# Performance work log

Hardware: AMD Instinct MI355X
Metric: run time of the kernel (lower is better)

## Reference

```python
import jax, jax.numpy as jnp
import numpy as np

EMBED_DIM = 1280
NUM_HEADS = 20
HEAD_DIM = EMBED_DIM // NUM_HEADS


def setup_inputs() -> dict:
    key = jax.random.key(0)
    ks = jax.random.split(key, 9)
    s = 0.02
    return {
        "hidden_states": jax.random.normal(ks[0], (4, 1500, EMBED_DIM), dtype=jnp.float32),
        "q_w": jax.random.normal(ks[1], (EMBED_DIM, EMBED_DIM), dtype=jnp.float32) * s,
        "q_b": jax.random.normal(ks[2], (EMBED_DIM,), dtype=jnp.float32) * s,
        "k_w": jax.random.normal(ks[3], (EMBED_DIM, EMBED_DIM), dtype=jnp.float32) * s,
        "v_w": jax.random.normal(ks[4], (EMBED_DIM, EMBED_DIM), dtype=jnp.float32) * s,
        "v_b": jax.random.normal(ks[5], (EMBED_DIM,), dtype=jnp.float32) * s,
        "o_w": jax.random.normal(ks[6], (EMBED_DIM, EMBED_DIM), dtype=jnp.float32) * s,
        "o_b": jax.random.normal(ks[7], (EMBED_DIM,), dtype=jnp.float32) * s,
    }


def reference(hidden_states, q_w, q_b, k_w, v_w, v_b, o_w, o_b):
    B, T, E = hidden_states.shape
    H, D = NUM_HEADS, HEAD_DIM
    scaling = D ** (-0.5)
    # projections (torch Linear: x @ W^T + b)
    q = (hidden_states @ q_w.T + q_b) * scaling
    k = hidden_states @ k_w.T  # k_proj has bias=False
    v = hidden_states @ v_w.T + v_b
    # [B, H, T, D]
    q = q.reshape(B, T, H, D).transpose(0, 2, 1, 3)
    k = k.reshape(B, T, H, D).transpose(0, 2, 1, 3)
    v = v.reshape(B, T, H, D).transpose(0, 2, 1, 3)
    # NOTE: module divides by sqrt(head_dim) AGAIN inside the kernel (faithful)
    scores = jnp.einsum("bhqd,bhkd->bhqk", q, k) / jnp.sqrt(jnp.asarray(D, q.dtype))
    attn = jax.nn.softmax(scores, axis=-1)
    out = jnp.einsum("bhqk,bhkd->bhqd", attn, v)
    out = out.transpose(0, 2, 1, 3).reshape(B, T, E)
    return out @ o_w.T + o_b
```

## Files before the change

### kernel.cpp

```cpp
#include <hip/hip_runtime.h>

typedef __attribute__((ext_vector_type(4))) float f32x4;
typedef __attribute__((ext_vector_type(8))) __bf16 bf16x8;
typedef __attribute__((ext_vector_type(4))) __bf16 bf16x4;

#define DEV __device__ __forceinline__

DEV f32x4 mfma_bf16(bf16x8 a, bf16x8 b, f32x4 c) {
  return __builtin_amdgcn_mfma_f32_16x16x32_bf16(a, b, c, 0, 0, 0);
}

DEV void glds16(const void* gp, void* lp) {
  __builtin_amdgcn_global_load_lds((const __attribute__((address_space(1))) void*)gp,
                                   (__attribute__((address_space(3))) void*)lp, 16, 0, 0);
}

DEV float fast_exp2(float x) {
#if __has_builtin(__builtin_amdgcn_exp2f)
  return __builtin_amdgcn_exp2f(x);
#else
  float r;
  asm("v_exp_f32 %0, %1" : "=v"(r) : "v"(x));
  return r;
#endif
}

#define SB0() __builtin_amdgcn_sched_barrier(0)

__global__ __launch_bounds__(256) void cvt_all(const float* __restrict__ hs,
                                               const float* __restrict__ qw,
                                               const float* __restrict__ kw,
                                               const float* __restrict__ vw,
                                               const float* __restrict__ ow,
                                               __bf16* __restrict__ oX,
                                               __bf16* __restrict__ oQ,
                                               __bf16* __restrict__ oK,
                                               __bf16* __restrict__ oV,
                                               __bf16* __restrict__ oO) {
  const int blk = blockIdx.x;
  if (blk < 3840) {
    long long e = ((long long)blk * 256 + threadIdx.x) * 8;
    bf16x8 o = {};
    if (e < 7680000) {
      const f32x4* ip = (const f32x4*)(hs + e);
      f32x4 a = ip[0], b = ip[1];
#pragma unroll
      for (int j = 0; j < 4; ++j) { o[j] = (__bf16)a[j]; o[j + 4] = (__bf16)b[j]; }
    }
    *(bf16x8*)(oX + e) = o;
  } else {
    const int wb = blk - 3840;
    const int which = wb / 800;
    const int bb = wb - which * 800;
    const float* in = which == 0 ? qw : which == 1 ? kw : which == 2 ? vw : ow;
    __bf16* out = which == 0 ? oQ : which == 1 ? oK : which == 2 ? oV : oO;
    long long e = ((long long)bb * 256 + threadIdx.x) * 8;
    const f32x4* ip = (const f32x4*)(in + e);
    f32x4 x = ip[0], y = ip[1];
    bf16x8 o;
#pragma unroll
    for (int j = 0; j < 4; ++j) { o[j] = (__bf16)x[j]; o[j + 4] = (__bf16)y[j]; }
    *(bf16x8*)(out + e) = o;
  }
}

__global__ __launch_bounds__(512, 4) void gemm_qkv(const __bf16* __restrict__ A,
                                                   const __bf16* __restrict__ Bw,
                                                   const float* __restrict__ qbias,
                                                   const float* __restrict__ vbias,
                                                   __bf16* __restrict__ Qo,
                                                   __bf16* __restrict__ Ko,
                                                   __bf16* __restrict__ Vto,
                                                   float sq) {
  __shared__ __align__(16) __bf16 lds[3 * 12288];
  const int tid = threadIdx.x;
  const int lane = tid & 63, wave = tid >> 6;
  const int wrow = wave >> 2, wcol = wave & 3;
  const int r = lane & 15, g = lane >> 4;

  const int orig = blockIdx.x;
  const int xcd = orig & 7, ii = orig >> 3;
  const int m_idx = xcd * 6 + ii % 6;
  const int n_idx = ii / 6;
  const int m0 = m_idx * 128, n0 = n_idx * 256;

  const f32x4 fz = {0.f, 0.f, 0.f, 0.f};
  f32x4 acc[4][4];
#pragma unroll
  for (int mi = 0; mi < 4; ++mi)
#pragma unroll
    for (int ni = 0; ni < 4; ++ni) acc[mi][ni] = fz;

  const __bf16* srcA0;
  const __bf16* srcB[2];
  {
    const int row = tid >> 2, ch = tid & 3;
    srcA0 = A + (size_t)(m0 + row) * 1280 + (ch ^ ((row >> 1) & 3)) * 8;
  }
#pragma unroll
  for (int j = 0; j < 2; ++j) {
    const int slot = j * 512 + tid;
    const int row = slot >> 2, ch = slot & 3;
    srcB[j] = Bw + (size_t)(n0 + row) * 1280 + (ch ^ ((row >> 1) & 3)) * 8;
  }
  const int wdst = wave * 512;

  auto stage = [&](int buf, int kt2) {
    const int k0 = kt2 * 32;
    __bf16* L = &lds[buf * 12288];
    glds16(srcA0 + k0, L + wdst);
    glds16(srcB[0] + k0, L + 4096 + wdst);
    glds16(srcB[1] + k0, L + 8192 + wdst);
  };

  stage(0, 0);
  stage(1, 1);
  asm volatile("s_waitcnt vmcnt(3)" ::: "memory");
  SB0();
  __builtin_amdgcn_s_barrier();
  SB0();

  const int aoff = (wrow * 64 + r) * 32;
  const int boff = 4096 + (wcol * 64 + r) * 32;
  const int csw = (g ^ ((r >> 1) & 3)) * 8;

  int cur = 0;
  for (int kt = 0; kt < 40; ++kt) {
    int nxt2 = cur + 2; if (nxt2 >= 3) nxt2 -= 3;
    const __bf16* Lb = &lds[cur * 12288];
    const bool pf = (kt + 2 < 40);

    bf16x8 af[4], bfr[4];
#pragma unroll
    for (int mi = 0; mi < 4; ++mi) af[mi] = *(const bf16x8*)&Lb[aoff + mi * 512 + csw];
#pragma unroll
    for (int ni = 0; ni < 4; ++ni) bfr[ni] = *(const bf16x8*)&Lb[boff + ni * 512 + csw];
    if (pf) stage(nxt2, kt + 2);
    asm volatile("s_waitcnt lgkmcnt(0)" ::: "memory");
    SB0();
    __builtin_amdgcn_s_setprio(1);
#pragma unroll
    for (int mi = 0; mi < 4; ++mi)
#pragma unroll
      for (int ni = 0; ni < 4; ++ni)
        acc[mi][ni] = mfma_bf16(af[mi], bfr[ni], acc[mi][ni]);
    __builtin_amdgcn_s_setprio(0);

    if (pf) asm volatile("s_waitcnt vmcnt(3)" ::: "memory");
    else    asm volatile("s_waitcnt vmcnt(0)" ::: "memory");
    SB0();
    __builtin_amdgcn_s_barrier();
    SB0();
    cur = cur + 1; if (cur >= 3) cur -= 3;
  }

  const int which = n_idx / 5;
  const int nb = n0 - which * 1280 + wcol * 64;
  const float scale = (which == 0) ? sq : 1.f;

#pragma unroll
  for (int ni = 0; ni < 4; ++ni) {
    const int col = nb + ni * 16 + r;
    const float bv = (which == 0) ? qbias[col] : (which == 2) ? vbias[col] : 0.f;
#pragma unroll
    for (int mi = 0; mi < 4; ++mi) {
      if (which == 2) {
        const int row0 = m0 + wrow * 64 + mi * 16 + g * 4;
        if (row0 < 6000) {
          const int bidx = row0 / 1500;
          const int t = row0 - bidx * 1500;
          union { __bf16 h[4]; unsigned long long u; } pk;
#pragma unroll
          for (int rr = 0; rr < 4; ++rr) pk.h[rr] = (__bf16)(acc[mi][ni][rr] + bv);
          *(unsigned long long*)&Vto[((size_t)(bidx * 1280 + col)) * 1536 + t] = pk.u;
        }
      } else {
        __bf16* dst = (which == 0) ? Qo : Ko;
#pragma unroll
        for (int rr = 0; rr < 4; ++rr) {
          const int row = m0 + wrow * 64 + mi * 16 + g * 4 + rr;
          dst[(size_t)row * 1280 + col] = (__bf16)((acc[mi][ni][rr] + bv) * scale);
        }
      }
    }
  }
}

__global__ __launch_bounds__(512, 2) void gemm_o(const __bf16* __restrict__ A,
                                                 const __bf16* __restrict__ Bw,
                                                 const float* __restrict__ bias,
                                                 float* __restrict__ out) {
  __shared__ __align__(16) __bf16 lds[3 * 24576];
  const int tid = threadIdx.x;
  const int lane = tid & 63, wave = tid >> 6;
  const int wrow = wave >> 2, wcol = wave & 3;
  const int r = lane & 15, g = lane >> 4;

  const int orig = blockIdx.x;
  const int xcd = orig & 7, ii = orig >> 3;
  const int m_idx = xcd * 6 + ii % 6;
  const int n_idx = ii / 6;
  const int m0 = m_idx * 128, n0 = n_idx * 256;

  const f32x4 fz = {0.f, 0.f, 0.f, 0.f};
  f32x4 acc[4][4];
#pragma unroll
  for (int mi = 0; mi < 4; ++mi)
#pragma unroll
    for (int ni = 0; ni < 4; ++ni) acc[mi][ni] = fz;

  const __bf16* srcA[2];
  const __bf16* srcB[4];
#pragma unroll
  for (int j = 0; j < 2; ++j) {
    const int slot = j * 512 + tid;
    const int row = slot >> 3, ch = slot & 7;
    srcA[j] = A + (size_t)(m0 + row) * 1280 + (ch ^ (row & 7)) * 8;
  }
#pragma unroll
  for (int j = 0; j < 4; ++j) {
    const int slot = j * 512 + tid;
    const int row = slot >> 3, ch = slot & 7;
    srcB[j] = Bw + (size_t)(n0 + row) * 1280 + (ch ^ (row & 7)) * 8;
  }
  const int wdst = wave * 512;

  auto stage_h0 = [&](int buf, int kt2) {
    const int k0 = kt2 * 64;
    glds16(srcA[0] + k0, &lds[buf * 24576 + wdst]);
    glds16(srcA[1] + k0, &lds[buf * 24576 + 4096 + wdst]);
    glds16(srcB[0] + k0, &lds[buf * 24576 + 8192 + wdst]);
  };
  auto stage_h1 = [&](int buf, int kt2) {
    const int k0 = kt2 * 64;
    glds16(srcB[1] + k0, &lds[buf * 24576 + 12288 + wdst]);
    glds16(srcB[2] + k0, &lds[buf * 24576 + 16384 + wdst]);
    glds16(srcB[3] + k0, &lds[buf * 24576 + 20480 + wdst]);
  };

  stage_h0(0, 0); stage_h1(0, 0);
  stage_h0(1, 1); stage_h1(1, 1);
  asm volatile("s_waitcnt vmcnt(6)" ::: "memory");
  SB0();
  __builtin_amdgcn_s_barrier();
  SB0();

  const int aoff = (wrow * 64 + r) * 64;
  const int boff = 8192 + (wcol * 64 + r) * 64;
  const int c0 = (g ^ (r & 7)) * 8;
  const int c1 = ((4 + g) ^ (r & 7)) * 8;

  int cur = 0;
  for (int kt = 0; kt < 20; ++kt) {
    int nxt2 = cur + 2; if (nxt2 >= 3) nxt2 -= 3;
    const __bf16* Lb = &lds[cur * 24576];
    const bool pf = (kt + 2 < 20);

    bf16x8 af[4], bfr[4];
#pragma unroll
    for (int mi = 0; mi < 4; ++mi) af[mi] = *(const bf16x8*)&Lb[aoff + mi * 1024 + c0];
#pragma unroll
    for (int ni = 0; ni < 4; ++ni) bfr[ni] = *(const bf16x8*)&Lb[boff + ni * 1024 + c0];
    if (pf) stage_h0(nxt2, kt + 2);
    asm volatile("s_waitcnt lgkmcnt(0)" ::: "memory");
    SB0();
    __builtin_amdgcn_s_setprio(1);
#pragma unroll
    for (int mi = 0; mi < 4; ++mi)
#pragma unroll
      for (int ni = 0; ni < 4; ++ni)
        acc[mi][ni] = mfma_bf16(af[mi], bfr[ni], acc[mi][ni]);
    __builtin_amdgcn_s_setprio(0);

    bf16x8 af1[4], bfr1[4];
#pragma unroll
    for (int mi = 0; mi < 4; ++mi) af1[mi] = *(const bf16x8*)&Lb[aoff + mi * 1024 + c1];
#pragma unroll
    for (int ni = 0; ni < 4; ++ni) bfr1[ni] = *(const bf16x8*)&Lb[boff + ni * 1024 + c1];
    if (pf) stage_h1(nxt2, kt + 2);
    asm volatile("s_waitcnt lgkmcnt(0)" ::: "memory");
    SB0();
    __builtin_amdgcn_s_setprio(1);
#pragma unroll
    for (int mi = 0; mi < 4; ++mi)
#pragma unroll
      for (int ni = 0; ni < 4; ++ni)
        acc[mi][ni] = mfma_bf16(af1[mi], bfr1[ni], acc[mi][ni]);
    __builtin_amdgcn_s_setprio(0);

    if (pf) asm volatile("s_waitcnt vmcnt(6)" ::: "memory");
    else    asm volatile("s_waitcnt vmcnt(0)" ::: "memory");
    SB0();
    __builtin_amdgcn_s_barrier();
    SB0();
    cur = cur + 1; if (cur >= 3) cur -= 3;
  }

#pragma unroll
  for (int ni = 0; ni < 4; ++ni) {
    const int col = n0 + wcol * 64 + ni * 16 + r;
    const float bv = bias[col];
#pragma unroll
    for (int mi = 0; mi < 4; ++mi) {
#pragma unroll
      for (int rr = 0; rr < 4; ++rr) {
        const int row = m0 + wrow * 64 + mi * 16 + g * 4 + rr;
        if (row < 6000) out[(size_t)row * 1280 + col] = acc[mi][ni][rr] + bv;
      }
    }
  }
}

__global__ __launch_bounds__(256, 2) void flash_attn(const __bf16* __restrict__ Qg,
                                                     const __bf16* __restrict__ Kg,
                                                     const __bf16* __restrict__ Vt,
                                                     __bf16* __restrict__ Og) {
  constexpr int TQ = 1500, NKT = 24;
  __shared__ __align__(16) __bf16 lds[18432];

  const int tid = threadIdx.x;
  const int lane = tid & 63, w = tid >> 6;
  const int r = lane & 15, g = lane >> 4;

  const int orig = blockIdx.x;
  const int work = (orig & 7) * 60 + (orig >> 3);
  const int bh = work / 6, qb = work - bh * 6;
  const int b = bh / 20, h = bh - b * 20;
  const int q0 = qb * 256;
  const size_t base = (size_t)b * (TQ * 1280) + h * 64;
  const __bf16* Vt_bh = Vt + (size_t)(b * 1280 + h * 64) * 1536;

  const int k_src_col = 8 * ((lane & 7) ^ (lane >> 3));
  const int k_row_loc = w * 8 + (lane >> 3);
  const int v_d_loc = 8 * w + (lane >> 3);
  const int v_chunk = 8 * ((lane & 7) ^ (lane >> 3));

  bf16x8 qf[4][2];
#pragma unroll
  for (int qs = 0; qs < 4; ++qs) {
    int t = q0 + w * 64 + qs * 16 + r;
    t = t < TQ ? t : TQ - 1;
    const __bf16* qp = Qg + base + (size_t)t * 1280;
#pragma unroll
    for (int dk = 0; dk < 2; ++dk) qf[qs][dk] = *(const bf16x8*)(qp + dk * 32 + g * 8);
  }

  bf16x8 ones;
#pragma unroll
  for (int j = 0; j < 8; ++j) ones[j] = (__bf16)1.0f;

  const f32x4 fz = {0.f, 0.f, 0.f, 0.f};
  f32x4 o_acc[4][4], o_sum[4];
#pragma unroll
  for (int qs = 0; qs < 4; ++qs) {
    o_sum[qs] = fz;
#pragma unroll
    for (int ni = 0; ni < 4; ++ni) o_acc[qs][ni] = fz;
  }

  auto stage = [&](int buf, int kt2) {
    const int kb = kt2 * 64;
#pragma unroll
    for (int i = 0; i < 2; ++i) {
      int row = kb + i * 32 + k_row_loc;
      row = row < TQ ? row : TQ - 1;
      glds16(Kg + base + (size_t)row * 1280 + k_src_col,
             &lds[buf * 8192 + i * 2048 + w * 512]);
    }
#pragma unroll
    for (int i = 0; i < 2; ++i) {
      glds16(Vt_bh + (size_t)(32 * i + v_d_loc) * 1536 + kb + v_chunk,
             &lds[buf * 8192 + 4096 + i * 2048 + w * 512]);
    }
  };

  stage(0, 0);
  __syncthreads();
  for (int kt = 0; kt < NKT; ++kt) {
    const int cur = kt & 1;
    if (kt + 1 < NKT) stage(cur ^ 1, kt + 1);

    const __bf16* Kb = &lds[cur * 8192];

    f32x4 s[4][4];
#pragma unroll
    for (int qs = 0; qs < 4; ++qs)
#pragma unroll
      for (int nt = 0; nt < 4; ++nt) s[qs][nt] = fz;
#pragma unroll
    for (int dk = 0; dk < 2; ++dk) {
      bf16x8 kf[4];
#pragma unroll
      for (int nt = 0; nt < 4; ++nt) {
        const int row = nt * 16 + r;
        const int sc = (dk * 32 + g * 8) ^ ((r & 7) << 3);
        kf[nt] = *(const bf16x8*)&Kb[row * 64 + sc];
      }
      __builtin_amdgcn_s_setprio(1);
#pragma unroll
      for (int qs = 0; qs < 4; ++qs)
#pragma unroll
        for (int nt = 0; nt < 4; ++nt) s[qs][nt] = mfma_bf16(kf[nt], qf[qs][dk], s[qs][nt]);
      __builtin_amdgcn_s_setprio(0);
    }

    if (kt == NKT - 1) {
#pragma unroll
      for (int nt = 0; nt < 4; ++nt)
#pragma unroll
        for (int rr = 0; rr < 4; ++rr) {
          const int key = kt * 64 + nt * 16 + g * 4 + rr;
          if (key >= TQ) {
#pragma unroll
            for (int qs = 0; qs < 4; ++qs) s[qs][nt][rr] = -1.0e30f;
          }
        }
    }

#pragma unroll
    for (int qs = 0; qs < 4; ++qs)
#pragma unroll
      for (int nt = 0; nt < 4; ++nt)
#pragma unroll
        for (int rr = 0; rr < 4; ++rr)
          s[qs][nt][rr] = fast_exp2(s[qs][nt][rr]);

    const __bf16* Vbuf = &lds[cur * 8192 + 4096];
    const int swz = (r & 7) << 3;
#pragma unroll
    for (int ks = 0; ks < 2; ++ks) {
      bf16x8 pa[4];
#pragma unroll
      for (int qs = 0; qs < 4; ++qs) {
        bf16x8 t;
#pragma unroll
        for (int j = 0; j < 4; ++j) {
          t[j] = (__bf16)s[qs][2 * ks][j];
          t[4 + j] = (__bf16)s[qs][2 * ks + 1][j];
        }
        pa[qs] = t;
      }
      const int o1 = (32 * ks + 4 * g) ^ swz;
      const int o2 = (32 * ks + 16 + 4 * g) ^ swz;
      __builtin_amdgcn_s_setprio(1);
#pragma unroll
      for (int qs = 0; qs < 4; ++qs) o_sum[qs] = mfma_bf16(ones, pa[qs], o_sum[qs]);
#pragma unroll
      for (int ni = 0; ni < 4; ++ni) {
        const int dbase = (16 * ni + r) * 64;
        union { bf16x4 hh[2]; bf16x8 v; } u;
        u.hh[0] = *(const bf16x4*)&Vbuf[dbase + o1];
        u.hh[1] = *(const bf16x4*)&Vbuf[dbase + o2];
#pragma unroll
        for (int qs = 0; qs < 4; ++qs) o_acc[qs][ni] = mfma_bf16(u.v, pa[qs], o_acc[qs][ni]);
      }
      __builtin_amdgcn_s_setprio(0);
    }

    __syncthreads();
  }

  float inv[4];
#pragma unroll
  for (int qs = 0; qs < 4; ++qs) inv[qs] = 1.0f / o_sum[qs][0];

  __bf16* Ob = &lds[w * 4608];
#pragma unroll
  for (int qs = 0; qs < 4; ++qs) {
#pragma unroll
    for (int ni = 0; ni < 4; ++ni)
#pragma unroll
      for (int rr = 0; rr < 4; ++rr)
        Ob[(qs * 16 + r) * 72 + ni * 16 + g * 4 + rr] = (__bf16)(o_acc[qs][ni][rr] * inv[qs]);
  }
  __syncthreads();
  const int qg = q0 + w * 64 + lane;
  if (qg < TQ) {
#pragma unroll
    for (int v = 0; v < 8; ++v) {
      const int c = v * 8;
      bf16x8 val = *(const bf16x8*)&lds[w * 4608 + lane * 72 + c];
      *(bf16x8*)&Og[base + (size_t)qg * 1280 + c] = val;
    }
  }
}

extern "C" void kernel_launch(void* const* d_in, const int* in_sizes, int n_in,
                              void* d_out, int out_size, void* d_ws, size_t ws_size,
                              hipStream_t stream) {
  const float* hs = (const float*)d_in[0];
  const float* qw = (const float*)d_in[1];
  const float* qb = (const float*)d_in[2];
  const float* kw = (const float*)d_in[3];
  const float* vw = (const float*)d_in[4];
  const float* vb = (const float*)d_in[5];
  const float* ow = (const float*)d_in[6];
  const float* ob = (const float*)d_in[7];

  const long long MP = 6144LL * 1280;
  const long long WE = 1280LL * 1280;
  __bf16* Xb = (__bf16*)d_ws;
  __bf16* Wq = Xb + MP;
  __bf16* Wk = Wq + WE;
  __bf16* Wv = Wk + WE;
  __bf16* Wo = Wv + WE;
  __bf16* Qb = Wo + WE;
  __bf16* Kb = Qb + MP;
  __bf16* Vtb = Kb + MP;
  __bf16* Ab = Xb;

  cvt_all<<<7040, 256, 0, stream>>>(hs, qw, kw, vw, ow, Xb, Wq, Wk, Wv, Wo);

  const float SQ = 1.4426950408889634f / 64.f;
  gemm_qkv<<<720, 512, 0, stream>>>(Xb, Wq, qb, vb, Qb, Kb, Vtb, SQ);

  flash_attn<<<480, 256, 0, stream>>>(Qb, Kb, Vtb, Ab);

  gemm_o<<<240, 512, 0, stream>>>(Ab, Wo, ob, (float*)d_out);
}
```

Before: 159.7 us.

## Enlarge QKV GEMM tile to 256x256 with split-half ping-pong LDS pipeline

The QKV projection GEMM moves from 128x256 tiles with a K-step of 32 to 256x256 tiles with a K-step of 64. The work is split into A/B halves in a two-stage LDS buffer, with fine-grained barriers so the loads of each half overlap the MFMA work on the other half. Larger tiles raise arithmetic intensity per LDS/global load and halve the grid to 360 blocks. In exchange, register pressure is higher (32 accumulators), occupancy drops to 2 blocks, and there are many more barriers per iteration.

```diff
diff --git a/kernel.cpp b/kernel.cpp
--- a/kernel.cpp
+++ b/kernel.cpp
@@ -26,6 +26,9 @@
 }
 
 #define SB0() __builtin_amdgcn_sched_barrier(0)
+#define LGKM0() asm volatile("s_waitcnt lgkmcnt(0)" ::: "memory")
+#define VMC(n) asm volatile("s_waitcnt vmcnt(" #n ")" ::: "memory")
+#define BAR() __builtin_amdgcn_s_barrier()
 
 __global__ __launch_bounds__(256) void cvt_all(const float* __restrict__ hs,
                                                const float* __restrict__ qw,
@@ -64,7 +67,7 @@
   }
 }
 
-__global__ __launch_bounds__(512, 4) void gemm_qkv(const __bf16* __restrict__ A,
+__global__ __launch_bounds__(512, 2) void gemm_qkv(const __bf16* __restrict__ A,
                                                    const __bf16* __restrict__ Bw,
                                                    const float* __restrict__ qbias,
                                                    const float* __restrict__ vbias,
@@ -72,7 +75,7 @@
                                                    __bf16* __restrict__ Ko,
                                                    __bf16* __restrict__ Vto,
                                                    float sq) {
-  __shared__ __align__(16) __bf16 lds[3 * 12288];
+  __shared__ __align__(16) __bf16 lds[65536];
   const int tid = threadIdx.x;
   const int lane = tid & 63, wave = tid >> 6;
   const int wrow = wave >> 2, wcol = wave & 3;
@@ -80,79 +83,125 @@
 
   const int orig = blockIdx.x;
   const int xcd = orig & 7, ii = orig >> 3;
-  const int m_idx = xcd * 6 + ii % 6;
-  const int n_idx = ii / 6;
-  const int m0 = m_idx * 128, n0 = n_idx * 256;
+  const int m_idx = xcd * 3 + ii % 3;
+  const int n_idx = ii / 3;
+  const int m0 = m_idx * 256, n0 = n_idx * 256;
 
   const f32x4 fz = {0.f, 0.f, 0.f, 0.f};
-  f32x4 acc[4][4];
-#pragma unroll
-  for (int mi = 0; mi < 4; ++mi)
+  f32x4 acc[8][4];
+#pragma unroll
+  for (int mi = 0; mi < 8; ++mi)
 #pragma unroll
     for (int ni = 0; ni < 4; ++ni) acc[mi][ni] = fz;
 
-  const __bf16* srcA0;
-  const __bf16* srcB[2];
-  {
-    const int row = tid >> 2, ch = tid & 3;
-    srcA0 = A + (size_t)(m0 + row) * 1280 + (ch ^ ((row >> 1) & 3)) * 8;
-  }
+  const __bf16 *pA0[2], *pA1[2], *pB0[2], *pB1[2];
 #pragma unroll
   for (int j = 0; j < 2; ++j) {
-    const int slot = j * 512 + tid;
-    const int row = slot >> 2, ch = slot & 3;
-    srcB[j] = Bw + (size_t)(n0 + row) * 1280 + (ch ^ ((row >> 1) & 3)) * 8;
-  }
-  const int wdst = wave * 512;
-
-  auto stage = [&](int buf, int kt2) {
-    const int k0 = kt2 * 32;
-    __bf16* L = &lds[buf * 12288];
-    glds16(srcA0 + k0, L + wdst);
-    glds16(srcB[0] + k0, L + 4096 + wdst);
-    glds16(srcB[1] + k0, L + 8192 + wdst);
+    const int s = j * 512 + tid;
+    const int row = s >> 3, ch = s & 7;
+    const int sw = (ch ^ (row & 7)) * 8;
+    const int ga = (row >> 6) * 128 + (row & 63);
+    pA0[j] = A + (size_t)(m0 + ga) * 1280 + sw;
+    pA1[j] = A + (size_t)(m0 + ga + 64) * 1280 + sw;
+    const int gb = (row >> 5) * 64 + (row & 31);
+    pB0[j] = Bw + (size_t)(n0 + gb) * 1280 + sw;
+    pB1[j] = Bw + (size_t)(n0 + gb + 32) * 1280 + sw;
+  }
+  const int wd = wave * 512;
+
+  auto stg = [&](int rb, const __bf16* const* p, int kt2) {
+    const int k0 = (kt2 < 20 ? kt2 : 19) * 64;
+    glds16(p[0] + k0, &lds[rb + wd]);
+    glds16(p[1] + k0, &lds[rb + 4096 + wd]);
   };
 
-  stage(0, 0);
-  stage(1, 1);
-  asm volatile("s_waitcnt vmcnt(3)" ::: "memory");
+  stg(0, pA0, 0); stg(8192, pA1, 0); stg(16384, pB0, 0); stg(24576, pB1, 0);
+  stg(32768, pA0, 1); stg(40960, pA1, 1); stg(49152, pB0, 1); stg(57344, pB1, 1);
+  VMC(0);
   SB0();
-  __builtin_amdgcn_s_barrier();
+  BAR();
   SB0();
 
-  const int aoff = (wrow * 64 + r) * 32;
-  const int boff = 4096 + (wcol * 64 + r) * 32;
-  const int csw = (g ^ ((r >> 1) & 3)) * 8;
-
-  int cur = 0;
-  for (int kt = 0; kt < 40; ++kt) {
-    int nxt2 = cur + 2; if (nxt2 >= 3) nxt2 -= 3;
-    const __bf16* Lb = &lds[cur * 12288];
-    const bool pf = (kt + 2 < 40);
-
-    bf16x8 af[4], bfr[4];
-#pragma unroll
-    for (int mi = 0; mi < 4; ++mi) af[mi] = *(const bf16x8*)&Lb[aoff + mi * 512 + csw];
-#pragma unroll
-    for (int ni = 0; ni < 4; ++ni) bfr[ni] = *(const bf16x8*)&Lb[boff + ni * 512 + csw];
-    if (pf) stage(nxt2, kt + 2);
-    asm volatile("s_waitcnt lgkmcnt(0)" ::: "memory");
-    SB0();
-    __builtin_amdgcn_s_setprio(1);
-#pragma unroll
-    for (int mi = 0; mi < 4; ++mi)
-#pragma unroll
-      for (int ni = 0; ni < 4; ++ni)
-        acc[mi][ni] = mfma_bf16(af[mi], bfr[ni], acc[mi][ni]);
-    __builtin_amdgcn_s_setprio(0);
-
-    if (pf) asm volatile("s_waitcnt vmcnt(3)" ::: "memory");
-    else    asm volatile("s_waitcnt vmcnt(0)" ::: "memory");
-    SB0();
-    __builtin_amdgcn_s_barrier();
-    SB0();
-    cur = cur + 1; if (cur >= 3) cur -= 3;
-  }
+  const int arow = (wrow * 64 + r) * 64;
+  const int brow = (wcol * 32 + r) * 64;
+  const int c0 = (g ^ (r & 7)) * 8;
+  const int c1 = ((4 + g) ^ (r & 7)) * 8;
+
+  bf16x8 AL[4][2], AH[4][2], Bf[2][2];
+
+#define RD_A(dst, base)                                                    \
+  _Pragma("unroll") for (int m4 = 0; m4 < 4; ++m4) {                       \
+    dst[m4][0] = *(const bf16x8*)&lds[(base) + arow + m4 * 1024 + c0];     \
+    dst[m4][1] = *(const bf16x8*)&lds[(base) + arow + m4 * 1024 + c1];     \
+  }
+#define RD_B(base)                                                         \
+  _Pragma("unroll") for (int n2 = 0; n2 < 2; ++n2) {                       \
+    Bf[n2][0] = *(const bf16x8*)&lds[(base) + brow + n2 * 1024 + c0];      \
+    Bf[n2][1] = *(const bf16x8*)&lds[(base) + brow + n2 * 1024 + c1];      \
+  }
+#define MM(mbase, nbase, Aop)                                              \
+  __builtin_amdgcn_s_setprio(1);                                           \
+  _Pragma("unroll") for (int m4 = 0; m4 < 4; ++m4)                         \
+  _Pragma("unroll") for (int n2 = 0; n2 < 2; ++n2)                         \
+  _Pragma("unroll") for (int dk = 0; dk < 2; ++dk)                         \
+      acc[(mbase) + m4][(nbase) + n2] =                                    \
+          mfma_bf16(Aop[m4][dk], Bf[n2][dk], acc[(mbase) + m4][(nbase) + n2]); \
+  __builtin_amdgcn_s_setprio(0);
+
+  for (int i = 0; i < 10; ++i) {
+    const int t1 = 2 * i + 1, t2 = 2 * i + 2, t3 = 2 * i + 3;
+
+    RD_A(AL, 0); RD_B(16384);
+    stg(57344, pB1, t1);
+    BAR(); LGKM0(); SB0();
+    MM(0, 0, AL);
+    BAR(); SB0();
+
+    RD_A(AH, 8192);
+    stg(0, pA0, t2);
+    BAR(); LGKM0(); SB0();
+    MM(4, 0, AH);
+    BAR(); SB0();
+
+    RD_B(24576);
+    stg(8192, pA1, t2);
+    BAR(); LGKM0(); SB0();
+    MM(4, 2, AH);
+    BAR(); SB0();
+
+    stg(16384, pB0, t2);
+    BAR(); LGKM0(); SB0();
+    MM(0, 2, AL);
+    VMC(4); SB0();
+    BAR(); SB0();
+
+    RD_A(AL, 32768); RD_B(49152);
+    stg(24576, pB1, t2);
+    BAR(); LGKM0(); SB0();
+    MM(0, 0, AL);
+    BAR(); SB0();
+
+    RD_A(AH, 40960);
+    stg(32768, pA0, t3);
+    BAR(); LGKM0(); SB0();
+    MM(4, 0, AH);
+    BAR(); SB0();
+
+    RD_B(57344);
+    stg(49152, pB0, t3);
+    BAR(); LGKM0(); SB0();
+    MM(4, 2, AH);
+    BAR(); SB0();
+
+    stg(40960, pA1, t3);
+    BAR(); LGKM0(); SB0();
+    MM(0, 2, AL);
+    VMC(4); SB0();
+    BAR(); SB0();
+  }
+#undef RD_A
+#undef RD_B
+#undef MM
 
   const int which = n_idx / 5;
   const int nb = n0 - which * 1280 + wcol * 64;
@@ -163,9 +212,9 @@
     const int col = nb + ni * 16 + r;
     const float bv = (which == 0) ? qbias[col] : (which == 2) ? vbias[col] : 0.f;
 #pragma unroll
-    for (int mi = 0; mi < 4; ++mi) {
+    for (int mi = 0; mi < 8; ++mi) {
       if (which == 2) {
-        const int row0 = m0 + wrow * 64 + mi * 16 + g * 4;
+        const int row0 = m0 + wrow * 128 + mi * 16 + g * 4;
         if (row0 < 6000) {
           const int bidx = row0 / 1500;
           const int t = row0 - bidx * 1500;
@@ -178,7 +227,7 @@
         __bf16* dst = (which == 0) ? Qo : Ko;
 #pragma unroll
         for (int rr = 0; rr < 4; ++rr) {
-          const int row = m0 + wrow * 64 + mi * 16 + g * 4 + rr;
+          const int row = m0 + wrow * 128 + mi * 16 + g * 4 + rr;
           dst[(size_t)row * 1280 + col] = (__bf16)((acc[mi][ni][rr] + bv) * scale);
         }
       }
@@ -240,9 +289,9 @@
 
   stage_h0(0, 0); stage_h1(0, 0);
   stage_h0(1, 1); stage_h1(1, 1);
-  asm volatile("s_waitcnt vmcnt(6)" ::: "memory");
+  VMC(6);
   SB0();
-  __builtin_amdgcn_s_barrier();
+  BAR();
   SB0();
 
   const int aoff = (wrow * 64 + r) * 64;
@@ -262,7 +311,7 @@
 #pragma unroll
     for (int ni = 0; ni < 4; ++ni) bfr[ni] = *(const bf16x8*)&Lb[boff + ni * 1024 + c0];
     if (pf) stage_h0(nxt2, kt + 2);
-    asm volatile("s_waitcnt lgkmcnt(0)" ::: "memory");
+    LGKM0();
     SB0();
     __builtin_amdgcn_s_setprio(1);
 #pragma unroll
@@ -278,7 +327,7 @@
 #pragma unroll
     for (int ni = 0; ni < 4; ++ni) bfr1[ni] = *(const bf16x8*)&Lb[boff + ni * 1024 + c1];
     if (pf) stage_h1(nxt2, kt + 2);
-    asm volatile("s_waitcnt lgkmcnt(0)" ::: "memory");
+    LGKM0();
     SB0();
     __builtin_amdgcn_s_setprio(1);
 #pragma unroll
@@ -288,10 +337,10 @@
         acc[mi][ni] = mfma_bf16(af1[mi], bfr1[ni], acc[mi][ni]);
     __builtin_amdgcn_s_setprio(0);
 
-    if (pf) asm volatile("s_waitcnt vmcnt(6)" ::: "memory");
-    else    asm volatile("s_waitcnt vmcnt(0)" ::: "memory");
+    if (pf) VMC(6);
+    else    VMC(0);
     SB0();
-    __builtin_amdgcn_s_barrier();
+    BAR();
     SB0();
     cur = cur + 1; if (cur >= 3) cur -= 3;
   }
@@ -512,7 +561,7 @@
   cvt_all<<<7040, 256, 0, stream>>>(hs, qw, kw, vw, ow, Xb, Wq, Wk, Wv, Wo);
 
   const float SQ = 1.4426950408889634f / 64.f;
-  gemm_qkv<<<720, 512, 0, stream>>>(Xb, Wq, qb, vb, Qb, Kb, Vtb, SQ);
+  gemm_qkv<<<360, 512, 0, stream>>>(Xb, Wq, qb, vb, Qb, Kb, Vtb, SQ);
 
   flash_attn<<<480, 256, 0, stream>>>(Qb, Kb, Vtb, Ab);
 
```

Result: slower. 198.4 us (+24.3%).
